# Optimization experiments

Measured on AMD Instinct MI355X. Metric: run time of the kernel, lower is better.

The kernel has to match this reference:

```python
import jax, jax.numpy as jnp
import numpy as np

B, S, D, H = 4, 2048, 1024, 16
DK = D // H

def setup_inputs() -> dict:
    key = jax.random.key(0)
    ks = jax.random.split(key, 11)
    sc = 1.0 / np.sqrt(D)
    return {
        "query": jax.random.normal(ks[0], (B, S, D), jnp.float32),
        "key": jax.random.normal(ks[1], (B, S, D), jnp.float32),
        "value": jax.random.normal(ks[2], (B, S, D), jnp.float32),
        "Wq": jax.random.normal(ks[3], (D, D), jnp.float32) * sc,
        "bq": jnp.zeros((D,), jnp.float32),
        "Wk": jax.random.normal(ks[4], (D, D), jnp.float32) * sc,
        "bk": jnp.zeros((D,), jnp.float32),
        "Wv": jax.random.normal(ks[5], (D, D), jnp.float32) * sc,
        "bv": jnp.zeros((D,), jnp.float32),
        "Wo": jax.random.normal(ks[6], (D, D), jnp.float32) * sc,
        "bo": jnp.zeros((D,), jnp.float32),
    }

def _mha(query, key, value, Wq, bq, Wk, bk, Wv, bv, Wo, bo):
    # in_linear{0,1,2}: y = x @ W.T + b  (MetaLinearLayer, weight [out,in])
    def proj(x, W, b):
        y = jnp.einsum('bsd,ed->bse', x, W) + b
        return y.reshape(B, S, H, DK).transpose(0, 2, 1, 3)  # [B,H,S,DK]
    q = proj(query, Wq, bq)
    k = proj(key, Wk, bk)
    v = proj(value, Wv, bv)
    # scores = QK^T / sqrt(d_k)  -> [B,H,S,S] (materialized as in original)
    scores = jnp.einsum('bhqd,bhkd->bhqk', q, k) / jnp.sqrt(jnp.float32(DK))
    p_attn = jax.nn.softmax(scores, axis=-1)
    # dropout is identity in eval/reference mode
    x = jnp.einsum('bhqk,bhkd->bhqd', p_attn, v)
    x = x.transpose(0, 2, 1, 3).reshape(B, S, D)
    return jnp.einsum('bsd,ed->bse', x, Wo) + bo

def reference(query, key, value, Wq, bq, Wk, bk, Wv, bv, Wo, bo):
    return _mha(query, key, value, Wq, bq, Wk, bk, Wv, bv, Wo, bo)
```

## Files before the change

### kernel.cpp

```cpp
#include <hip/hip_runtime.h>
#include <stdint.h>

typedef __attribute__((ext_vector_type(4))) float f32x4;
typedef __attribute__((ext_vector_type(8))) __bf16 bf16x8;
typedef __attribute__((ext_vector_type(8))) unsigned short u16x8;
typedef __attribute__((ext_vector_type(4))) uint32_t u32x4;

#define GLOBAL_AS __attribute__((address_space(1)))
#define LDS_AS    __attribute__((address_space(3)))

__device__ __forceinline__ void lds_load16(const void* g, void* l) {
  __builtin_amdgcn_global_load_lds((const GLOBAL_AS uint32_t*)(uintptr_t)g,
                                   (LDS_AS uint32_t*)(uintptr_t)l, 16, 0, 0);
}

__device__ __forceinline__ unsigned short f2bf(float f) {
  uint32_t u = __builtin_bit_cast(uint32_t, f);
  u += 0x7fffu + ((u >> 16) & 1u);
  return (unsigned short)(u >> 16);
}

__device__ __forceinline__ uint32_t pk_bf16(float a, float b) {
#if __has_builtin(__builtin_amdgcn_cvt_pk_bf16_f32)
  return __builtin_bit_cast(uint32_t, __builtin_amdgcn_cvt_pk_bf16_f32(a, b));
#else
  return (uint32_t)f2bf(a) | ((uint32_t)f2bf(b) << 16);
#endif
}

__device__ __forceinline__ float exp2f_fast(float x) {
#if __has_builtin(__builtin_amdgcn_exp2f)
  return __builtin_amdgcn_exp2f(x);
#else
  return __expf(x * 0.6931471805599453f);
#endif
}

__device__ __forceinline__ bf16x8 pack8(const f32x4 a, const f32x4 b) {
  u32x4 d;
  d.x = pk_bf16(a[0], a[1]);
  d.y = pk_bf16(a[2], a[3]);
  d.z = pk_bf16(b[0], b[1]);
  d.w = pk_bf16(b[2], b[3]);
  return __builtin_bit_cast(bf16x8, d);
}

#define QK_SCALE 0.18033688011112042f

__global__ void cast_all(const float* __restrict__ q, const float* __restrict__ k,
                         const float* __restrict__ v, const float* __restrict__ Wq,
                         const float* __restrict__ Wk, const float* __restrict__ Wv,
                         const float* __restrict__ Wo, unsigned short* __restrict__ dst) {
  const int bid = blockIdx.x;
  const float* src;
  int rel;
  if (bid < 24576) {
    const int seg = bid >> 13;
    rel = bid & 8191;
    src = (seg == 0) ? q : (seg == 1) ? k : v;
  } else {
    const int w = (bid - 24576) >> 10;
    rel = (bid - 24576) & 1023;
    src = (w == 0) ? Wq : (w == 1) ? Wk : (w == 2) ? Wv : Wo;
  }
  const size_t di = (size_t)bid * 1024 + threadIdx.x * 4;
  const size_t si = (size_t)rel * 1024 + threadIdx.x * 4;
  const float4 val = *(const float4*)(src + si);
  ushort4 o;
  o.x = f2bf(val.x); o.y = f2bf(val.y); o.z = f2bf(val.z); o.w = f2bf(val.w);
  *(ushort4*)(dst + di) = o;
}

__global__ __launch_bounds__(256, 2)
void gemm_qkv(const unsigned short* __restrict__ xq, const unsigned short* __restrict__ xk,
              const unsigned short* __restrict__ xv, const unsigned short* __restrict__ wq,
              const unsigned short* __restrict__ wk, const unsigned short* __restrict__ wv,
              const float* __restrict__ bq, const float* __restrict__ bk,
              const float* __restrict__ bv,
              unsigned short* __restrict__ Qh, unsigned short* __restrict__ Kh,
              unsigned short* __restrict__ Vt)
{
  __shared__ __align__(16) unsigned short As[128 * 64];
  __shared__ __align__(16) unsigned short Bs[128 * 64];

  const int gy = blockIdx.y, gx = blockIdx.x;
  const unsigned short* A  = (gy == 0) ? xq : (gy == 1) ? xk : wv;
  const unsigned short* Bw = (gy == 0) ? wq : (gy == 1) ? wk : xv;
  const float* bias        = (gy == 0) ? bq : (gy == 1) ? bk : bv;

  int m0, n0, N;
  if (gy < 2) { m0 = (gx >> 3) * 128; n0 = (gx & 7) * 128; N = 1024; }
  else        { m0 = (gx & 7) * 128;  n0 = (gx >> 3) * 128; N = 8192; }
  const int K = 1024;

  const int tid  = threadIdx.x;
  const int wave = tid >> 6;
  const int lane = tid & 63;
  const int wm = wave >> 1, wn = wave & 1;
  const int quad = lane >> 4, l15 = lane & 15;

  f32x4 acc[4][4];
#pragma unroll
  for (int i = 0; i < 4; ++i)
#pragma unroll
    for (int j = 0; j < 4; ++j) acc[i][j] = f32x4{0.f, 0.f, 0.f, 0.f};

  const int sr8 = lane >> 3;
  const int scx = ((lane & 7) ^ (sr8 & 7)) * 8;
  const unsigned short* Agb = A  + (size_t)(m0 + wave * 8 + sr8) * K + scx;
  const unsigned short* Bgb = Bw + (size_t)(n0 + wave * 8 + sr8) * K + scx;
  unsigned short* AsW = &As[wave * 8 * 64];
  unsigned short* BsW = &Bs[wave * 8 * 64];

  const int colx0 = (quad * 8) ^ ((l15 & 7) * 8);
  const int colx1 = (32 + quad * 8) ^ ((l15 & 7) * 8);

  for (int k0 = 0; k0 < K; k0 += 64) {
#pragma unroll
    for (int t = 0; t < 4; ++t) {
      lds_load16(Agb + (size_t)(t * 32) * K + k0, AsW + t * 32 * 64);
      lds_load16(Bgb + (size_t)(t * 32) * K + k0, BsW + t * 32 * 64);
    }
    __syncthreads();

#pragma unroll
    for (int kd = 0; kd < 2; ++kd) {
      const int colx = kd ? colx1 : colx0;
      bf16x8 af[4], bfr[4];
#pragma unroll
      for (int i = 0; i < 4; ++i)
        af[i] = *(const bf16x8*)&As[(wm * 64 + i * 16 + l15) * 64 + colx];
#pragma unroll
      for (int j = 0; j < 4; ++j)
        bfr[j] = *(const bf16x8*)&Bs[(wn * 64 + j * 16 + l15) * 64 + colx];
#pragma unroll
      for (int i = 0; i < 4; ++i)
#pragma unroll
        for (int j = 0; j < 4; ++j)
          acc[i][j] = __builtin_amdgcn_mfma_f32_16x16x32_bf16(af[i], bfr[j], acc[i][j], 0, 0, 0);
    }
    __syncthreads();
  }

  if (gy < 2) {
    unsigned short* out = (gy == 0) ? Qh : Kh;
    const float scl = (gy == 0) ? QK_SCALE : 1.0f;
    float bj[4];
#pragma unroll
    for (int j = 0; j < 4; ++j) bj[j] = bias[n0 + wn * 64 + j * 16 + l15];
#pragma unroll
    for (int i = 0; i < 4; ++i) {
      const int mbase = m0 + wm * 64 + i * 16 + quad * 4;
#pragma unroll
      for (int j = 0; j < 4; ++j) {
        const int n = n0 + wn * 64 + j * 16 + l15;
#pragma unroll
        for (int r = 0; r < 4; ++r) {
          const int m = mbase + r;
          const float vv = (acc[i][j][r] + bj[j]) * scl;
          const size_t idx = ((((size_t)(m >> 11) * 16 + (n >> 6)) << 11) + (size_t)(m & 2047)) * 64 + (n & 63);
          out[idx] = f2bf(vv);
        }
      }
    }
  } else {
#pragma unroll
    for (int i = 0; i < 4; ++i) {
      const int mbase = m0 + wm * 64 + i * 16 + quad * 4;
      float bm[4];
#pragma unroll
      for (int r = 0; r < 4; ++r) bm[r] = bias[mbase + r];
#pragma unroll
      for (int j = 0; j < 4; ++j) {
        const int n = n0 + wn * 64 + j * 16 + l15;
#pragma unroll
        for (int r = 0; r < 4; ++r)
          Vt[(size_t)(mbase + r) * N + n] = f2bf(acc[i][j][r] + bm[r]);
      }
    }
  }
}

__global__ __launch_bounds__(256, 2)
void flash_attn(const unsigned short* __restrict__ Qh,
                const unsigned short* __restrict__ Kh,
                const unsigned short* __restrict__ VtG,
                unsigned short* __restrict__ Xo)
{
  __shared__ __align__(16) unsigned short Ks[128 * 72];
  __shared__ __align__(16) unsigned short Vs[64 * 136];

  const int fid = blockIdx.x + (blockIdx.y << 4) + (blockIdx.z << 8);
  const int wid = ((fid & 7) << 7) + (fid >> 3);
  const int qb = wid & 15, h = (wid >> 4) & 15, b = wid >> 8;

  const int tid = threadIdx.x, wave = tid >> 6, lane = tid & 63;
  const int quad = lane >> 4, l15 = lane & 15;

  const size_t bh = (((size_t)b * 16 + h) << 17);
  const unsigned short* Qg = Qh + bh + ((size_t)qb << 13);
  const unsigned short* Kg = Kh + bh;
  const unsigned short* Vg = VtG + ((size_t)(h * 64)) * 8192 + (size_t)b * 2048;

#pragma unroll
  for (int p = 0; p < 4; ++p) {
    const int c = tid + p * 256;
    u16x8 qv = *(const u16x8*)(Qg + c * 8);
    *(u16x8*)&Ks[(c >> 3) * 72 + (c & 7) * 8] = qv;
  }
  __syncthreads();
  bf16x8 aq[2][2];
#pragma unroll
  for (int i = 0; i < 2; ++i)
#pragma unroll
    for (int d = 0; d < 2; ++d)
      aq[i][d] = *(const bf16x8*)&Ks[(wave * 32 + i * 16 + l15) * 72 + d * 32 + quad * 8];

  f32x4 oacc[2][4];
  f32x4 lacc[2];
#pragma unroll
  for (int i = 0; i < 2; ++i) {
#pragma unroll
    for (int jd = 0; jd < 4; ++jd) oacc[i][jd] = f32x4{0.f, 0.f, 0.f, 0.f};
    lacc[i] = f32x4{0.f, 0.f, 0.f, 0.f};
  }

  const uint32_t one2 = 0x3F803F80u;
  const u32x4 onesU{one2, one2, one2, one2};
  const bf16x8 onesB = __builtin_bit_cast(bf16x8, onesU);

  const int rb = (l15 >> 3) * 16 + ((l15 >> 2) & 1) * 4 + (l15 & 3);

  u16x8 kreg[4], vreg[4];
#pragma unroll
  for (int p = 0; p < 4; ++p) {
    const int c = tid + p * 256;
    kreg[p] = *(const u16x8*)(Kg + c * 8);
    vreg[p] = *(const u16x8*)(Vg + (size_t)(c >> 4) * 8192 + (c & 15) * 8);
  }

  for (int kb = 0; kb < 16; ++kb) {
    __syncthreads();
#pragma unroll
    for (int p = 0; p < 4; ++p) {
      const int c = tid + p * 256;
      const int kr = c >> 3;
      const int krp = (kr & ~12) | ((kr & 4) << 1) | ((kr & 8) >> 1);
      *(u16x8*)&Ks[krp * 72 + (c & 7) * 8] = kreg[p];
      *(u16x8*)&Vs[(c >> 4) * 136 + (c & 15) * 8] = vreg[p];
    }
    __syncthreads();

#pragma unroll 1
    for (int hh = 0; hh < 2; ++hh) {
      f32x4 s[2][4];
#pragma unroll
      for (int i = 0; i < 2; ++i)
#pragma unroll
        for (int j = 0; j < 4; ++j) s[i][j] = f32x4{0.f, 0.f, 0.f, 0.f};
      __builtin_amdgcn_s_setprio(1);
#pragma unroll
      for (int d = 0; d < 2; ++d)
#pragma unroll
        for (int j = 0; j < 4; ++j) {
          const int kk = j >> 1, p2 = j & 1;
          bf16x8 kf = *(const bf16x8*)&Ks[(hh * 64 + kk * 32 + p2 * 8 + rb) * 72 + d * 32 + quad * 8];
#pragma unroll
          for (int i = 0; i < 2; ++i)
            s[i][j] = __builtin_amdgcn_mfma_f32_16x16x32_bf16(kf, aq[i][d], s[i][j], 0, 0, 0);
        }
      __builtin_amdgcn_s_setprio(0);

#pragma unroll
      for (int i = 0; i < 2; ++i)
#pragma unroll
        for (int j = 0; j < 4; ++j)
#pragma unroll
          for (int r = 0; r < 4; ++r)
            s[i][j][r] = exp2f_fast(s[i][j][r]);

      bf16x8 ap[2][2];
#pragma unroll
      for (int i = 0; i < 2; ++i)
#pragma unroll
        for (int kk = 0; kk < 2; ++kk)
          ap[i][kk] = pack8(s[i][2 * kk], s[i][2 * kk + 1]);

      if (kb < 15) {
        if (hh == 0) {
          const size_t ko = ((size_t)(kb + 1) << 13);
#pragma unroll
          for (int p = 0; p < 4; ++p) {
            const int c = tid + p * 256;
            kreg[p] = *(const u16x8*)(Kg + ko + c * 8);
          }
        } else {
#pragma unroll
          for (int p = 0; p < 4; ++p) {
            const int c = tid + p * 256;
            vreg[p] = *(const u16x8*)(Vg + (size_t)(c >> 4) * 8192 + (kb + 1) * 128 + (c & 15) * 8);
          }
        }
      }

      __builtin_amdgcn_s_setprio(1);
#pragma unroll
      for (int i = 0; i < 2; ++i)
#pragma unroll
        for (int kk = 0; kk < 2; ++kk)
          lacc[i] = __builtin_amdgcn_mfma_f32_16x16x32_bf16(ap[i][kk], onesB, lacc[i], 0, 0, 0);
#pragma unroll
      for (int kk = 0; kk < 2; ++kk) {
#pragma unroll
        for (int jd = 0; jd < 4; ++jd) {
          bf16x8 bv = *(const bf16x8*)&Vs[(jd * 16 + l15) * 136 + (hh * 2 + kk) * 32 + quad * 8];
#pragma unroll
          for (int i = 0; i < 2; ++i)
            oacc[i][jd] = __builtin_amdgcn_mfma_f32_16x16x32_bf16(ap[i][kk], bv, oacc[i][jd], 0, 0, 0);
        }
      }
      __builtin_amdgcn_s_setprio(0);
    }
  }

#pragma unroll
  for (int i = 0; i < 2; ++i)
#pragma unroll
    for (int r = 0; r < 4; ++r) {
      const float inv = 1.f / lacc[i][r];
      const int srow = qb * 128 + wave * 32 + i * 16 + quad * 4 + r;
      const size_t obase = (((size_t)b << 11) + srow) * 1024 + (h << 6);
#pragma unroll
      for (int jd = 0; jd < 4; ++jd)
        Xo[obase + jd * 16 + l15] = f2bf(oacc[i][jd][r] * inv);
    }
}

__global__ __launch_bounds__(256, 2)
void gemm_out(const unsigned short* __restrict__ A,
              const unsigned short* __restrict__ Bw,
              const float* __restrict__ bias,
              float* __restrict__ Cout)
{
  __shared__ __align__(16) unsigned short As[128 * 64];
  __shared__ __align__(16) unsigned short Bs[128 * 64];

  const int tid  = threadIdx.x;
  const int wave = tid >> 6;
  const int lane = tid & 63;
  const int wm = wave >> 1, wn = wave & 1;
  const int quad = lane >> 4, l15 = lane & 15;
  const int m0 = blockIdx.y * 128;
  const int n0 = blockIdx.x * 128;
  const int K = 1024, N = 1024;

  f32x4 acc[4][4];
#pragma unroll
  for (int i = 0; i < 4; ++i)
#pragma unroll
    for (int j = 0; j < 4; ++j) acc[i][j] = f32x4{0.f, 0.f, 0.f, 0.f};

  const int sr8 = lane >> 3;
  const int scx = ((lane & 7) ^ (sr8 & 7)) * 8;
  const unsigned short* Agb = A  + (size_t)(m0 + wave * 8 + sr8) * K + scx;
  const unsigned short* Bgb = Bw + (size_t)(n0 + wave * 8 + sr8) * K + scx;
  unsigned short* AsW = &As[wave * 8 * 64];
  unsigned short* BsW = &Bs[wave * 8 * 64];

  const int colx0 = (quad * 8) ^ ((l15 & 7) * 8);
  const int colx1 = (32 + quad * 8) ^ ((l15 & 7) * 8);

  for (int k0 = 0; k0 < K; k0 += 64) {
#pragma unroll
    for (int t = 0; t < 4; ++t) {
      lds_load16(Agb + (size_t)(t * 32) * K + k0, AsW + t * 32 * 64);
      lds_load16(Bgb + (size_t)(t * 32) * K + k0, BsW + t * 32 * 64);
    }
    __syncthreads();

#pragma unroll
    for (int kd = 0; kd < 2; ++kd) {
      const int colx = kd ? colx1 : colx0;
      bf16x8 af[4], bfr[4];
#pragma unroll
      for (int i = 0; i < 4; ++i)
        af[i] = *(const bf16x8*)&As[(wm * 64 + i * 16 + l15) * 64 + colx];
#pragma unroll
      for (int j = 0; j < 4; ++j)
        bfr[j] = *(const bf16x8*)&Bs[(wn * 64 + j * 16 + l15) * 64 + colx];
#pragma unroll
      for (int i = 0; i < 4; ++i)
#pragma unroll
        for (int j = 0; j < 4; ++j)
          acc[i][j] = __builtin_amdgcn_mfma_f32_16x16x32_bf16(af[i], bfr[j], acc[i][j], 0, 0, 0);
    }
    __syncthreads();
  }

  float bj[4];
#pragma unroll
  for (int j = 0; j < 4; ++j) bj[j] = bias[n0 + wn * 64 + j * 16 + l15];

#pragma unroll
  for (int i = 0; i < 4; ++i) {
    const int mbase = m0 + wm * 64 + i * 16 + quad * 4;
#pragma unroll
    for (int j = 0; j < 4; ++j) {
      const int n = n0 + wn * 64 + j * 16 + l15;
#pragma unroll
      for (int r = 0; r < 4; ++r)
        Cout[(size_t)(mbase + r) * N + n] = acc[i][j][r] + bj[j];
    }
  }
}

extern "C" void kernel_launch(void* const* d_in, const int* in_sizes, int n_in,
                              void* d_out, int out_size, void* d_ws, size_t ws_size,
                              hipStream_t stream) {
  const float* q  = (const float*)d_in[0];
  const float* k  = (const float*)d_in[1];
  const float* v  = (const float*)d_in[2];
  const float* Wq = (const float*)d_in[3];
  const float* bq = (const float*)d_in[4];
  const float* Wk = (const float*)d_in[5];
  const float* bk = (const float*)d_in[6];
  const float* Wv = (const float*)d_in[7];
  const float* bv = (const float*)d_in[8];
  const float* Wo = (const float*)d_in[9];
  const float* bo = (const float*)d_in[10];

  const int B = 4, S = 2048, D = 1024, H = 16;
  const size_t NX = (size_t)B * S * D;
  const size_t NW = (size_t)D * D;

  unsigned short* xq = (unsigned short*)d_ws;
  unsigned short* xk = xq + NX;
  unsigned short* xv = xk + NX;
  unsigned short* wq = xv + NX;
  unsigned short* wk = wq + NW;
  unsigned short* wv = wk + NW;
  unsigned short* wo = wv + NW;
  unsigned short* Qh = wo + NW;
  unsigned short* Kh = Qh + NX;
  unsigned short* Vt = Kh + NX;
  unsigned short* xo = Vt + NX;

  cast_all<<<28672, 256, 0, stream>>>(q, k, v, Wq, Wk, Wv, Wo, xq);
  gemm_qkv<<<dim3(512, 3), 256, 0, stream>>>(xq, xk, xv, wq, wk, wv, bq, bk, bv, Qh, Kh, Vt);
  flash_attn<<<dim3(S / 128, H, B), 256, 0, stream>>>(Qh, Kh, Vt, xo);
  gemm_out<<<dim3(D / 128, (B * S) / 128), 256, 0, stream>>>(xo, wo, bo, (float*)d_out);
}
```

Measured before the change: 344.2 us.

## Fuse activation fp32-to-bf16 cast into QKV GEMM tile loads

Stops casting the query/key/value activations to bf16 in a separate pass and converts them on the fly inside the QKV projection GEMM. The GEMM reads fp32 rows with vector loads, packs them to bf16 and writes them into the swizzled LDS tile, while weights still use async global-to-LDS loads. This removes a full read and write of three large activation tensors and one launch's worth of work. In exchange the GEMM reads twice the bytes per activation tile from global memory through registers, losing async LDS loading for that operand, and any 8x reuse of each activation tile across N-blocks now repeats the conversion.

```diff
diff --git a/kernel.cpp b/kernel.cpp
--- a/kernel.cpp
+++ b/kernel.cpp
@@ -47,22 +47,13 @@
 
 #define QK_SCALE 0.18033688011112042f
 
-__global__ void cast_all(const float* __restrict__ q, const float* __restrict__ k,
-                         const float* __restrict__ v, const float* __restrict__ Wq,
-                         const float* __restrict__ Wk, const float* __restrict__ Wv,
-                         const float* __restrict__ Wo, unsigned short* __restrict__ dst) {
+__global__ void cast_all(const float* __restrict__ Wq, const float* __restrict__ Wk,
+                         const float* __restrict__ Wv, const float* __restrict__ Wo,
+                         unsigned short* __restrict__ dst) {
   const int bid = blockIdx.x;
-  const float* src;
-  int rel;
-  if (bid < 24576) {
-    const int seg = bid >> 13;
-    rel = bid & 8191;
-    src = (seg == 0) ? q : (seg == 1) ? k : v;
-  } else {
-    const int w = (bid - 24576) >> 10;
-    rel = (bid - 24576) & 1023;
-    src = (w == 0) ? Wq : (w == 1) ? Wk : (w == 2) ? Wv : Wo;
-  }
+  const int w = bid >> 10;
+  const int rel = bid & 1023;
+  const float* src = (w == 0) ? Wq : (w == 1) ? Wk : (w == 2) ? Wv : Wo;
   const size_t di = (size_t)bid * 1024 + threadIdx.x * 4;
   const size_t si = (size_t)rel * 1024 + threadIdx.x * 4;
   const float4 val = *(const float4*)(src + si);
@@ -72,9 +63,10 @@
 }
 
 __global__ __launch_bounds__(256, 2)
-void gemm_qkv(const unsigned short* __restrict__ xq, const unsigned short* __restrict__ xk,
-              const unsigned short* __restrict__ xv, const unsigned short* __restrict__ wq,
-              const unsigned short* __restrict__ wk, const unsigned short* __restrict__ wv,
+void gemm_qkv(const float* __restrict__ qf, const float* __restrict__ kf,
+              const float* __restrict__ vf,
+              const unsigned short* __restrict__ wq, const unsigned short* __restrict__ wk,
+              const unsigned short* __restrict__ wv,
               const float* __restrict__ bq, const float* __restrict__ bk,
               const float* __restrict__ bv,
               unsigned short* __restrict__ Qh, unsigned short* __restrict__ Kh,
@@ -84,14 +76,19 @@
   __shared__ __align__(16) unsigned short Bs[128 * 64];
 
   const int gy = blockIdx.y, gx = blockIdx.x;
-  const unsigned short* A  = (gy == 0) ? xq : (gy == 1) ? xk : wv;
-  const unsigned short* Bw = (gy == 0) ? wq : (gy == 1) ? wk : xv;
-  const float* bias        = (gy == 0) ? bq : (gy == 1) ? bk : bv;
+  const float* F             = (gy == 0) ? qf : (gy == 1) ? kf : vf;
+  const unsigned short* Wb   = (gy == 0) ? wq : (gy == 1) ? wk : wv;
+  const float* bias          = (gy == 0) ? bq : (gy == 1) ? bk : bv;
 
   int m0, n0, N;
   if (gy < 2) { m0 = (gx >> 3) * 128; n0 = (gx & 7) * 128; N = 1024; }
   else        { m0 = (gx & 7) * 128;  n0 = (gx >> 3) * 128; N = 8192; }
   const int K = 1024;
+
+  const int frow0 = (gy < 2) ? m0 : n0;
+  const int wrow0 = (gy < 2) ? n0 : m0;
+  unsigned short* Ts = (gy < 2) ? As : Bs;
+  unsigned short* Us = (gy < 2) ? Bs : As;
 
   const int tid  = threadIdx.x;
   const int wave = tid >> 6;
@@ -107,19 +104,35 @@
 
   const int sr8 = lane >> 3;
   const int scx = ((lane & 7) ^ (sr8 & 7)) * 8;
-  const unsigned short* Agb = A  + (size_t)(m0 + wave * 8 + sr8) * K + scx;
-  const unsigned short* Bgb = Bw + (size_t)(n0 + wave * 8 + sr8) * K + scx;
-  unsigned short* AsW = &As[wave * 8 * 64];
-  unsigned short* BsW = &Bs[wave * 8 * 64];
+  const unsigned short* Wgb = Wb + (size_t)(wrow0 + wave * 8 + sr8) * K + scx;
+  unsigned short* UsW = &Us[wave * 8 * 64];
+
+  const int fr = wave * 8 + sr8;
+  const int pchunk = lane & 7;
+  const int schunk = pchunk ^ (sr8 & 7);
+  const float* Fgb = F + (size_t)(frow0 + fr) * K + schunk * 8;
+  unsigned short* TsW = &Ts[fr * 64 + pchunk * 8];
 
   const int colx0 = (quad * 8) ^ ((l15 & 7) * 8);
   const int colx1 = (32 + quad * 8) ^ ((l15 & 7) * 8);
 
   for (int k0 = 0; k0 < K; k0 += 64) {
 #pragma unroll
-    for (int t = 0; t < 4; ++t) {
-      lds_load16(Agb + (size_t)(t * 32) * K + k0, AsW + t * 32 * 64);
-      lds_load16(Bgb + (size_t)(t * 32) * K + k0, BsW + t * 32 * 64);
+    for (int t = 0; t < 4; ++t)
+      lds_load16(Wgb + (size_t)(t * 32) * K + k0, UsW + t * 32 * 64);
+#pragma unroll
+    for (int th = 0; th < 2; ++th) {
+      float4 v0a = *(const float4*)(Fgb + (size_t)((th * 2 + 0) * 32) * K + k0);
+      float4 v1a = *(const float4*)(Fgb + (size_t)((th * 2 + 0) * 32) * K + k0 + 4);
+      float4 v0b = *(const float4*)(Fgb + (size_t)((th * 2 + 1) * 32) * K + k0);
+      float4 v1b = *(const float4*)(Fgb + (size_t)((th * 2 + 1) * 32) * K + k0 + 4);
+      u32x4 da, db;
+      da.x = pk_bf16(v0a.x, v0a.y); da.y = pk_bf16(v0a.z, v0a.w);
+      da.z = pk_bf16(v1a.x, v1a.y); da.w = pk_bf16(v1a.z, v1a.w);
+      db.x = pk_bf16(v0b.x, v0b.y); db.y = pk_bf16(v0b.z, v0b.w);
+      db.z = pk_bf16(v1b.x, v1b.y); db.w = pk_bf16(v1b.z, v1b.w);
+      *(u32x4*)(TsW + (th * 2 + 0) * 32 * 64) = da;
+      *(u32x4*)(TsW + (th * 2 + 1) * 32 * 64) = db;
     }
     __syncthreads();
 
@@ -445,8 +458,11 @@
   unsigned short* Vt = Kh + NX;
   unsigned short* xo = Vt + NX;
 
-  cast_all<<<28672, 256, 0, stream>>>(q, k, v, Wq, Wk, Wv, Wo, xq);
-  gemm_qkv<<<dim3(512, 3), 256, 0, stream>>>(xq, xk, xv, wq, wk, wv, bq, bk, bv, Qh, Kh, Vt);
+  cast_all<<<4096, 256, 0, stream>>>(Wq, Wk, Wv, Wo, wq);
+
+  gemm_qkv<<<dim3(512, 3), 256, 0, stream>>>(q, k, v, wq, wk, wv, bq, bk, bv, Qh, Kh, Vt);
+
   flash_attn<<<dim3(S / 128, H, B), 256, 0, stream>>>(Qh, Kh, Vt, xo);
+
   gemm_out<<<dim3(D / 128, (B * S) / 128), 256, 0, stream>>>(xo, wo, bo, (float*)d_out);
 }
```

After: 409.8 us. +19.1%, slower.
